# Optimization experiments

Measured on AMD Instinct MI355X. Metric: run time of the kernel, lower is better.

The kernel has to match this reference:

```python
import jax, jax.numpy as jnp
import numpy as np

MARGIN = 0.0


def setup_inputs() -> dict:
    key = jax.random.key(0)
    k1, k2, k3 = jax.random.split(key, 3)
    n, d = 8192, 128
    inputs = jax.random.normal(k1, (n, d), dtype=jnp.float32)
    targets = jax.random.randint(k2, (n,), 0, 512, dtype=jnp.int64)
    cids = jax.random.randint(k3, (n,), 0, 8, dtype=jnp.int64)
    return {"inputs": inputs, "targets": targets, "cids": cids}


def _margin_ranking_loss(x1, x2, margin):
    # nn.MarginRankingLoss with y=1: mean(max(0, -(x1 - x2) + margin))
    return jnp.mean(jnp.maximum(x2 - x1 + margin, 0.0))


def reference(inputs, targets, cids):
    n = inputs.shape[0]
    # pairwise euclidean distance matrix [n, n]
    sq = jnp.sum(inputs * inputs, axis=1)              # [n]
    d2 = sq[:, None] + sq[None, :] - 2.0 * (inputs @ inputs.T)
    dist = jnp.sqrt(jnp.clip(d2, 1e-12, 1e12))         # [n, n]

    mask = targets[:, None] == targets[None, :]        # [n, n] same-identity
    # view_mask (cids) is computed in the original but never used

    # hardest positive (max over same-id, incl. self) and hardest negative (min over diff-id)
    pos_masked = jnp.where(mask, dist, -jnp.inf)
    neg_masked = jnp.where(mask, jnp.inf, dist)
    dist_ap = jnp.max(pos_masked, axis=1)              # [n]
    dist_an = jnp.min(neg_masked, axis=1)              # [n]
    p2_ind = jnp.argmax(pos_masked, axis=1)            # [n]
    n1_ind = jnp.argmin(neg_masked, axis=1)            # [n]

    # secondary neighbors: hardest-negative of the hardest negative,
    # hardest-positive of the hardest positive (row lookups)
    dist_n12 = dist_an[n1_ind]                         # min of dist[n1_ind] over ~mask[n1_ind]
    dist_p12 = dist_ap[p2_ind]                         # max of dist[p2_ind] over mask[p2_ind]

    loss = (_margin_ranking_loss(dist_an, dist_ap, MARGIN)
            + 0.1 * _margin_ranking_loss(dist_n12, dist_ap, MARGIN)
            + 0.1 * _margin_ranking_loss(dist_an, dist_p12, MARGIN))
    prec = jnp.mean((dist_an > dist_ap).astype(jnp.float32))
    return loss, prec, dist
```

## Files before the change

kernel.cpp:

```cpp
#include <hip/hip_runtime.h>

#define NROWS 8192
#define DDIM 128

typedef unsigned short u16;
typedef unsigned int u32;
typedef unsigned long long u64;
typedef __attribute__((ext_vector_type(4))) float f32x4;
typedef __attribute__((ext_vector_type(2))) float f32x2;
typedef __attribute__((ext_vector_type(4))) int i32x4;
typedef __attribute__((ext_vector_type(8))) short short8;

__device__ __forceinline__ u16 f32_to_bf16(float f){
  u32 u = __float_as_uint(f);
  u32 r = (u + 0x7FFFu + ((u >> 16) & 1u)) >> 16;
  return (u16)r;
}
__device__ __forceinline__ float bf16_to_f32(u16 h){ return __uint_as_float(((u32)h) << 16); }

__global__ __launch_bounds__(256) void pack_kernel(const float* __restrict__ in,
                                                   u16* __restrict__ phi, u16* __restrict__ plo,
                                                   float* __restrict__ sq){
  int t = blockIdx.x * 256 + threadIdx.x;
  int r = t >> 4, s = t & 15;
  const float* src = in + (size_t)r * DDIM + s * 8;
  f32x4 a = *(const f32x4*)(src);
  f32x4 b = *(const f32x4*)(src + 4);
  float x[8] = {a.x, a.y, a.z, a.w, b.x, b.y, b.z, b.w};
  short8 hv, lv;
  float ss = 0.f;
  #pragma unroll
  for (int j = 0; j < 8; ++j){
    u16 h = f32_to_bf16(x[j]);
    u16 l = f32_to_bf16(x[j] - bf16_to_f32(h));
    hv[j] = (short)h; lv[j] = (short)l;
    ss += x[j] * x[j];
  }
  size_t dst = (((size_t)(r >> 4) * 4 + (s >> 2)) * 64 + (s & 3) * 16 + (r & 15)) * 8;
  *(short8*)(phi + dst) = hv;
  *(short8*)(plo + dst) = lv;
  #pragma unroll
  for (int m = 1; m < 16; m <<= 1) ss += __shfl_xor(ss, m, 64);
  if (s == 0) sq[r] = ss;
}

__global__ __launch_bounds__(256, 3) void dist_kernel(
    const u16* __restrict__ phi, const u16* __restrict__ plo,
    const float* __restrict__ sq, const int* __restrict__ tgt,
    float* __restrict__ dist, u64* __restrict__ pos_key, u64* __restrict__ neg_key)
{
  int id = blockIdx.x;
  int swz = (id & 7) * 512 + (id >> 3);
  const int bi = swz >> 6, bj = swz & 63;

  const int tid = threadIdx.x;
  const int w = tid >> 6, lane = tid & 63;
  const int wr = w >> 1, wc = w & 1;
  const int lr = lane & 15, g = lane >> 4;

  f32x4 acc[4][4] = {};

  #pragma unroll
  for (int kk = 0; kk < 4; ++kk){
    short8 ah[4], al[4], bh[4], bl[4];
    #pragma unroll
    for (int m = 0; m < 4; ++m){
      size_t offA = ((size_t)(((bi * 8 + wr * 4 + m) * 4 + kk) * 64) + lane) * 8;
      ah[m] = *(const short8*)(phi + offA);
      al[m] = *(const short8*)(plo + offA);
      size_t offB = ((size_t)(((bj * 8 + wc * 4 + m) * 4 + kk) * 64) + lane) * 8;
      bh[m] = *(const short8*)(phi + offB);
      bl[m] = *(const short8*)(plo + offB);
    }
    #pragma unroll
    for (int m = 0; m < 4; ++m)
      #pragma unroll
      for (int n = 0; n < 4; ++n){
        acc[m][n] = __builtin_amdgcn_mfma_f32_16x16x32_bf16(bh[n], ah[m], acc[m][n], 0, 0, 0);
        acc[m][n] = __builtin_amdgcn_mfma_f32_16x16x32_bf16(bl[n], ah[m], acc[m][n], 0, 0, 0);
        acc[m][n] = __builtin_amdgcn_mfma_f32_16x16x32_bf16(bh[n], al[m], acc[m][n], 0, 0, 0);
      }
  }

  f32x4 sqc[4]; i32x4 tcv[4]; int cbase[4];
  #pragma unroll
  for (int n = 0; n < 4; ++n){
    cbase[n] = bj * 128 + wc * 64 + n * 16 + g * 4;
    sqc[n] = *(const f32x4*)(sq + cbase[n]);
    tcv[n] = *(const i32x4*)(tgt + cbase[n]);
  }
  #pragma unroll
  for (int m = 0; m < 4; ++m){
    const int grow = bi * 128 + wr * 64 + m * 16 + lr;
    const float sqr = sq[grow];
    const int tr = tgt[grow];
    float bpv = -1.f, bnv = 3.0e38f; int bpc = 0x7FFFFFFF, bnc = 0x7FFFFFFF;
    float* drow = dist + (size_t)grow * NROWS;
    #pragma unroll
    for (int n = 0; n < 4; ++n){
      f32x4 dd4;
      #pragma unroll
      for (int r = 0; r < 4; ++r){
        float d2 = sqr + sqc[n][r] - 2.f * acc[m][n][r];
        d2 = fminf(fmaxf(d2, 1e-12f), 1e12f);
        float dd = sqrtf(d2);
        dd4[r] = dd;
        if (tr == tcv[n][r]){
          if (dd > bpv){ bpv = dd; bpc = cbase[n] + r; }
        } else {
          if (dd < bnv){ bnv = dd; bnc = cbase[n] + r; }
        }
      }
      *(f32x2*)(drow + cbase[n])     = f32x2{dd4.x, dd4.y};
      *(f32x2*)(drow + cbase[n] + 2) = f32x2{dd4.z, dd4.w};
    }
    #pragma unroll
    for (int msk = 16; msk <= 32; msk <<= 1){
      float ov = __shfl_xor(bpv, msk, 64); int oc = __shfl_xor(bpc, msk, 64);
      if (ov > bpv || (ov == bpv && oc < bpc)){ bpv = ov; bpc = oc; }
      ov = __shfl_xor(bnv, msk, 64); oc = __shfl_xor(bnc, msk, 64);
      if (ov < bnv || (ov == bnv && oc < bnc)){ bnv = ov; bnc = oc; }
    }
    if (g == 0){
      if (bpv >= 0.f)
        atomicMax(&pos_key[grow],
                  ((u64)__float_as_uint(bpv) << 32) | (u64)(0xFFFFFFFFu - (u32)bpc));
      if (bnv < 3.0e38f)
        atomicMin(&neg_key[grow],
                  ((u64)__float_as_uint(bnv) << 32) | (u64)(u32)bnc);
    }
  }
}

__global__ __launch_bounds__(256) void decode_kernel(const u64* __restrict__ pk, const u64* __restrict__ nk,
                                                     float* __restrict__ ap, float* __restrict__ an,
                                                     int* __restrict__ p2, int* __restrict__ n1){
  int i = blockIdx.x * 256 + threadIdx.x;
  u64 p = pk[i], q = nk[i];
  ap[i] = __uint_as_float((u32)(p >> 32));
  p2[i] = (int)(0xFFFFFFFFu - (u32)(p & 0xFFFFFFFFu));
  an[i] = __uint_as_float((u32)(q >> 32));
  n1[i] = (int)(u32)(q & 0xFFFFFFFFu);
}

__global__ __launch_bounds__(256) void final_kernel(const float* __restrict__ ap, const float* __restrict__ an,
                                                    const int* __restrict__ p2, const int* __restrict__ n1,
                                                    float* __restrict__ out){
  __shared__ float r1[256], r2[256], r3[256]; __shared__ int r4[256];
  int tid = threadIdx.x;
  float s1 = 0.f, s2 = 0.f, s3 = 0.f; int pc = 0;
  for (int i = tid; i < NROWS; i += 256){
    float a = ap[i], b = an[i];
    float n12 = an[n1[i]];
    float p12 = ap[p2[i]];
    s1 += fmaxf(a - b, 0.f);
    s2 += fmaxf(a - n12, 0.f);
    s3 += fmaxf(p12 - b, 0.f);
    pc += (b > a) ? 1 : 0;
  }
  r1[tid] = s1; r2[tid] = s2; r3[tid] = s3; r4[tid] = pc;
  __syncthreads();
  for (int s = 128; s > 0; s >>= 1){
    if (tid < s){ r1[tid] += r1[tid + s]; r2[tid] += r2[tid + s]; r3[tid] += r3[tid + s]; r4[tid] += r4[tid + s]; }
    __syncthreads();
  }
  if (tid == 0){
    float inv = 1.f / (float)NROWS;
    out[0] = r1[0] * inv + 0.1f * (r2[0] * inv) + 0.1f * (r3[0] * inv);
    out[1] = (float)r4[0] * inv;
  }
}

extern "C" void kernel_launch(void* const* d_in, const int* in_sizes, int n_in,
                              void* d_out, int out_size, void* d_ws, size_t ws_size,
                              hipStream_t stream){
  const float* inputs = (const float*)d_in[0];
  const int* targets = (const int*)d_in[1];
  float* out = (float*)d_out;
  char* ws = (char*)d_ws;

  u16* phi = (u16*)ws;
  u16* plo = (u16*)(ws + (2u << 20));
  float* sq = (float*)(ws + (4u << 20));
  u64* pos_key = (u64*)(ws + (4u << 20) + (64u << 10));
  u64* neg_key = (u64*)(ws + (4u << 20) + (128u << 10));
  float* ap = (float*)(ws + (4u << 20) + (192u << 10));
  float* an = (float*)(ws + (4u << 20) + (224u << 10));
  int* p2 = (int*)(ws + (4u << 20) + (256u << 10));
  int* n1 = (int*)(ws + (4u << 20) + (288u << 10));

  hipMemsetAsync(pos_key, 0x00, NROWS * sizeof(u64), stream);
  hipMemsetAsync(neg_key, 0xFF, NROWS * sizeof(u64), stream);

  pack_kernel<<<(NROWS * 16) / 256, 256, 0, stream>>>(inputs, phi, plo, sq);
  dist_kernel<<<64 * 64, 256, 0, stream>>>(phi, plo, sq, targets, out + 2, pos_key, neg_key);
  decode_kernel<<<NROWS / 256, 256, 0, stream>>>(pos_key, neg_key, ap, an, p2, n1);
  final_kernel<<<1, 256, 0, stream>>>(ap, an, p2, n1, out);
}
```

Before: 157.7 us.

## Exploit distance symmetry by computing only upper-triangle tiles and transposing via LDS

The dist kernel now launches only the 2080 upper-triangular 128x128 tiles and maps each block index to a (bi, bj) pair with bj >= bi. Each off-diagonal tile is staged in shared memory, then written a second time transposed into the mirrored position, and the hardest positive/negative reductions are also done for the mirrored rows. This roughly halves the MFMA work while the full dist matrix still gets written. The cost is a 66 KB LDS buffer per block, lower occupancy (launch bounds 3 to 2), an extra barrier, and transpose reads from LDS.

```diff
diff --git a/kernel.cpp b/kernel.cpp
--- a/kernel.cpp
+++ b/kernel.cpp
@@ -1,4 +1,5 @@
 #include <hip/hip_runtime.h>
+#include <math.h>
 
 #define NROWS 8192
 #define DDIM 128
@@ -44,16 +45,26 @@
   if (s == 0) sq[r] = ss;
 }
 
-__global__ __launch_bounds__(256, 3) void dist_kernel(
+__global__ __launch_bounds__(256, 2) void dist_kernel(
     const u16* __restrict__ phi, const u16* __restrict__ plo,
     const float* __restrict__ sq, const int* __restrict__ tgt,
     float* __restrict__ dist, u64* __restrict__ pos_key, u64* __restrict__ neg_key)
 {
+  __shared__ float ldsC[128 * 129];
+  __shared__ int s_trow[128];
+
   int id = blockIdx.x;
-  int swz = (id & 7) * 512 + (id >> 3);
-  const int bi = swz >> 6, bj = swz & 63;
+  int swz = (id & 7) * 260 + (id >> 3);
+  int bi = (int)((129.0 - sqrt(16641.0 - 8.0 * (double)swz)) * 0.5);
+  bi = bi < 0 ? 0 : (bi > 63 ? 63 : bi);
+  int tbase = bi * 64 - (bi * (bi - 1)) / 2;
+  while (swz < tbase) { --bi; tbase = bi * 64 - (bi * (bi - 1)) / 2; }
+  while (swz >= tbase + (64 - bi)) { tbase += (64 - bi); ++bi; }
+  const int bj = bi + (swz - tbase);
 
   const int tid = threadIdx.x;
+  if (tid < 128) s_trow[tid] = tgt[bi * 128 + tid];
+
   const int w = tid >> 6, lane = tid & 63;
   const int wr = w >> 1, wc = w & 1;
   const int lr = lane & 15, g = lane >> 4;
@@ -91,13 +102,16 @@
   }
   #pragma unroll
   for (int m = 0; m < 4; ++m){
-    const int grow = bi * 128 + wr * 64 + m * 16 + lr;
+    const int row128 = wr * 64 + m * 16 + lr;
+    const int grow = bi * 128 + row128;
     const float sqr = sq[grow];
     const int tr = tgt[grow];
     float bpv = -1.f, bnv = 3.0e38f; int bpc = 0x7FFFFFFF, bnc = 0x7FFFFFFF;
     float* drow = dist + (size_t)grow * NROWS;
+    float* lrow = ldsC + row128 * 129;
     #pragma unroll
     for (int n = 0; n < 4; ++n){
+      const int col128 = wc * 64 + n * 16 + g * 4;
       f32x4 dd4;
       #pragma unroll
       for (int r = 0; r < 4; ++r){
@@ -105,6 +119,7 @@
         d2 = fminf(fmaxf(d2, 1e-12f), 1e12f);
         float dd = sqrtf(d2);
         dd4[r] = dd;
+        lrow[col128 + r] = dd;
         if (tr == tcv[n][r]){
           if (dd > bpv){ bpv = dd; bpc = cbase[n] + r; }
         } else {
@@ -127,6 +142,42 @@
                   ((u64)__float_as_uint(bpv) << 32) | (u64)(0xFFFFFFFFu - (u32)bpc));
       if (bnv < 3.0e38f)
         atomicMin(&neg_key[grow],
+                  ((u64)__float_as_uint(bnv) << 32) | (u64)(u32)bnc);
+    }
+  }
+
+  __syncthreads();
+
+  if (bi != bj){
+    const int c = tid >> 1, half = tid & 1;
+    const int orow = bj * 128 + c;
+    const int tc = tgt[orow];
+    float bpv = -1.f, bnv = 3.0e38f; int bpc = 0x7FFFFFFF, bnc = 0x7FFFFFFF;
+    float* drow = dist + (size_t)orow * NROWS + bi * 128 + half * 64;
+    const int r0base = half * 64;
+    #pragma unroll 8
+    for (int i = 0; i < 64; i += 2){
+      int r0 = r0base + i;
+      float d0 = ldsC[(r0)     * 129 + c];
+      float d1 = ldsC[(r0 + 1) * 129 + c];
+      *(f32x2*)(drow + i) = f32x2{d0, d1};
+      int gc0 = bi * 128 + r0;
+      int t0 = s_trow[r0], t1 = s_trow[r0 + 1];
+      if (t0 == tc){ if (d0 > bpv){ bpv = d0; bpc = gc0; } }
+      else         { if (d0 < bnv){ bnv = d0; bnc = gc0; } }
+      if (t1 == tc){ if (d1 > bpv){ bpv = d1; bpc = gc0 + 1; } }
+      else         { if (d1 < bnv){ bnv = d1; bnc = gc0 + 1; } }
+    }
+    float ov = __shfl_xor(bpv, 1, 64); int oc = __shfl_xor(bpc, 1, 64);
+    if (ov > bpv || (ov == bpv && oc < bpc)){ bpv = ov; bpc = oc; }
+    ov = __shfl_xor(bnv, 1, 64); oc = __shfl_xor(bnc, 1, 64);
+    if (ov < bnv || (ov == bnv && oc < bnc)){ bnv = ov; bnc = oc; }
+    if (half == 0){
+      if (bpv >= 0.f)
+        atomicMax(&pos_key[orow],
+                  ((u64)__float_as_uint(bpv) << 32) | (u64)(0xFFFFFFFFu - (u32)bpc));
+      if (bnv < 3.0e38f)
+        atomicMin(&neg_key[orow],
                   ((u64)__float_as_uint(bnv) << 32) | (u64)(u32)bnc);
     }
   }
@@ -193,7 +244,7 @@
   hipMemsetAsync(neg_key, 0xFF, NROWS * sizeof(u64), stream);
 
   pack_kernel<<<(NROWS * 16) / 256, 256, 0, stream>>>(inputs, phi, plo, sq);
-  dist_kernel<<<64 * 64, 256, 0, stream>>>(phi, plo, sq, targets, out + 2, pos_key, neg_key);
+  dist_kernel<<<2080, 256, 0, stream>>>(phi, plo, sq, targets, out + 2, pos_key, neg_key);
   decode_kernel<<<NROWS / 256, 256, 0, stream>>>(pos_key, neg_key, ap, an, p2, n1);
   final_kernel<<<1, 256, 0, stream>>>(ap, an, p2, n1, out);
 }
```

New measurement: 268.9 us. 70.4% more time.
